# Optimization experiments

Measured on AMD Instinct MI355X. Metric: run time of the kernel, lower is better.

The kernel has to match this reference:

```python
import jax, jax.numpy as jnp
import numpy as np

NH = 16
D = 1024
B, T = 4, 4096


def setup_inputs() -> dict:
    key = jax.random.key(0)
    k1, k2, k3, k4 = jax.random.split(key, 4)
    x = jax.random.normal(k1, (B, T, D), dtype=jnp.float32)
    phi = jax.random.normal(k2, (B, T), dtype=jnp.float32)
    W_attn = jax.random.normal(k3, (D, D), dtype=jnp.float32) * 0.02
    W_proj = jax.random.normal(k4, (D, D), dtype=jnp.float32) * 0.02
    gamma = jnp.ones((NH, 1), dtype=jnp.float32)
    temp = jnp.ones((NH, 1), dtype=jnp.float32)
    return {"x": x, "phi": phi, "W_attn": W_attn, "W_proj": W_proj,
            "gamma": gamma, "temp": temp}


def reference(x, phi, W_attn, W_proj, gamma, temp):
    Bb, Tt, d = x.shape
    hd = d // NH
    # c_attn (no bias), split heads: [B, nh, T, hd]
    w = (x @ W_attn.T).reshape(Bb, Tt, NH, hd).transpose(0, 2, 1, 3)
    w_sq = w * w
    denom = jnp.maximum(jnp.cumsum(w_sq, axis=-2), 1e-12)
    w_norm = w_sq / denom
    tssa_score = w_norm.sum(-1) * temp                       # [B, nh, T]
    phi_Q = phi[:, None, :]                                  # [B, 1, T]
    steps = jnp.arange(1, Tt + 1, dtype=x.dtype)
    mean_phi = jnp.cumsum(phi, axis=-1)[:, None, :] / steps  # running mean of phi
    penalty = (phi_Q - mean_phi) ** 2                        # [B, 1, T]
    score = tssa_score - gamma * penalty                     # [B, nh, T]
    alpha = jax.nn.softmax(score, axis=1)                    # softmax over HEADS (dim=1)
    dots = jnp.cumsum(w_sq * alpha[..., None], axis=-2) / (
        jnp.cumsum(alpha, axis=-1)[..., None] + 1e-8)
    attn = jnp.minimum(1.0 / (1.0 + dots), 10000.0)
    y = -w * alpha[..., None] * attn                          # [B, nh, T, hd]
    y = y.transpose(0, 2, 1, 3).reshape(Bb, Tt, d)
    y = y @ W_proj.T                                          # dropout is identity (p=0 / eval)
    return (y, alpha)
```

## Files before the change

kernel.cpp:

```cpp
#include <hip/hip_runtime.h>
#include <hip/hip_bf16.h>
#include <stdint.h>

#define NHh 16
#define Dm  1024
#define HD  64
#define Bb  4
#define Tt  4096
#define NCH 128
#define CHL 32

#define BM 256
#define BN 256
#define BK 64
#define NKT (Dm / BK)

using bf16 = __hip_bfloat16;
typedef __attribute__((ext_vector_type(8))) short short8;
typedef __attribute__((ext_vector_type(4))) float f32x4;

__device__ __forceinline__ float bf2f(bf16 v) { return __bfloat162float(v); }

__device__ __forceinline__ float b2f(unsigned short u) {
  union { unsigned int i; float f; } x; x.i = ((unsigned int)u) << 16; return x.f;
}

__device__ __forceinline__ float frcp(float x) {
  float r; asm("v_rcp_f32 %0, %1" : "=v"(r) : "v"(x)); return r;
}

__device__ __forceinline__ void gld_lds16(const void* g, void* l) {
  __builtin_amdgcn_global_load_lds(
      (const __attribute__((address_space(1))) unsigned int*)g,
      (__attribute__((address_space(3))) unsigned int*)l, 16, 0, 0);
}

template <bool OUT_BF16, bool WRITE_S1>
__global__ __launch_bounds__(512, 2) void gemm256(const bf16* __restrict__ A,
                                                  const bf16* __restrict__ W,
                                                  void* __restrict__ Cout,
                                                  float* __restrict__ S1,
                                                  int M, int N, int K) {
  extern __shared__ char smem[];
  const int tid  = threadIdx.x;
  const int lane = tid & 63;
  const int wave = tid >> 6;
  const int bid = blockIdx.x;
  const int swz = (bid & 7) * 32 + (bid >> 3);
  const int bn = (swz & 3) * BN;
  const int bm = (swz >> 2) * BM;
  const int wm = (wave >> 1) * 64;
  const int wn = (wave & 1) * 128;
  const int quad = lane >> 4;
  const int l16  = lane & 15;

  const int srow = wave * 8 + (lane >> 3);
  const int scol = (((lane & 7) ^ (lane >> 3)) << 3);

  const bf16* Abase = A + (size_t)(bm + srow) * K + scol;
  const bf16* Wbase = W + (size_t)(bn + srow) * K + scol;

  f32x4 acc[4][8] = {};

#define SLAB_A(buf, n) (smem + (buf) * 65536 + (n) * 8192 + wave * 1024)
#define SLAB_B(buf, n) (smem + (buf) * 65536 + 32768 + (n) * 8192 + wave * 1024)
#define STAGE_A(buf, n, k0) gld_lds16(Abase + (size_t)(n) * 64 * K + (k0), SLAB_A(buf, n))
#define STAGE_B(buf, n, k0) gld_lds16(Wbase + (size_t)(n) * 64 * K + (k0), SLAB_B(buf, n))
#define LD_FRAG(base, r, s) (*(const short8*)((base) + (size_t)(r) * 128 + ((((s) ^ ((r) & 7))) << 4)))

  STAGE_A(0, 0, 0); STAGE_A(0, 1, 0); STAGE_A(0, 2, 0); STAGE_A(0, 3, 0);
  STAGE_B(0, 0, 0); STAGE_B(0, 1, 0); STAGE_B(0, 2, 0); STAGE_B(0, 3, 0);
  asm volatile("s_waitcnt vmcnt(0)" ::: "memory");
  __builtin_amdgcn_s_barrier();
  __builtin_amdgcn_sched_barrier(0);

  short8 af[4][2], bfv[4][2];
  for (int t = 0; t < NKT; t++) {
    const int buf = t & 1;
    const char* aL = smem + buf * 65536;
    const char* bL = aL + 32768;
    const int k0n = (t + 1) * BK;
    const bool pf = (t + 1 < NKT);

    if (pf) {
      STAGE_A(buf ^ 1, 0, k0n); STAGE_A(buf ^ 1, 1, k0n);
      STAGE_A(buf ^ 1, 2, k0n); STAGE_A(buf ^ 1, 3, k0n);
      STAGE_B(buf ^ 1, 0, k0n); STAGE_B(buf ^ 1, 2, k0n);
    }
#pragma unroll
    for (int mi = 0; mi < 4; mi++) {
      const int r = wm + mi * 16 + l16;
      af[mi][0] = LD_FRAG(aL, r, quad);
      af[mi][1] = LD_FRAG(aL, r, quad + 4);
    }
#pragma unroll
    for (int nj = 0; nj < 4; nj++) {
      const int r = wn + nj * 16 + l16;
      bfv[nj][0] = LD_FRAG(bL, r, quad);
      bfv[nj][1] = LD_FRAG(bL, r, quad + 4);
    }
    __builtin_amdgcn_s_setprio(1);
#pragma unroll
    for (int mi = 0; mi < 4; mi++)
#pragma unroll
      for (int nj = 0; nj < 4; nj++) {
        acc[mi][nj] = __builtin_amdgcn_mfma_f32_16x16x32_bf16(af[mi][0], bfv[nj][0], acc[mi][nj], 0, 0, 0);
        acc[mi][nj] = __builtin_amdgcn_mfma_f32_16x16x32_bf16(af[mi][1], bfv[nj][1], acc[mi][nj], 0, 0, 0);
      }
    __builtin_amdgcn_s_setprio(0);
    if (pf) { asm volatile("s_waitcnt vmcnt(6)" ::: "memory"); }
    else    { asm volatile("s_waitcnt vmcnt(0)" ::: "memory"); }
    __builtin_amdgcn_s_barrier();
    __builtin_amdgcn_sched_barrier(0);

    if (pf) { STAGE_B(buf ^ 1, 1, k0n); STAGE_B(buf ^ 1, 3, k0n); }
#pragma unroll
    for (int nj = 0; nj < 4; nj++) {
      const int r = wn + 64 + nj * 16 + l16;
      bfv[nj][0] = LD_FRAG(bL, r, quad);
      bfv[nj][1] = LD_FRAG(bL, r, quad + 4);
    }
    __builtin_amdgcn_s_setprio(1);
#pragma unroll
    for (int mi = 0; mi < 4; mi++)
#pragma unroll
      for (int nj = 0; nj < 4; nj++) {
        acc[mi][nj + 4] = __builtin_amdgcn_mfma_f32_16x16x32_bf16(af[mi][0], bfv[nj][0], acc[mi][nj + 4], 0, 0, 0);
        acc[mi][nj + 4] = __builtin_amdgcn_mfma_f32_16x16x32_bf16(af[mi][1], bfv[nj][1], acc[mi][nj + 4], 0, 0, 0);
      }
    __builtin_amdgcn_s_setprio(0);
    asm volatile("s_waitcnt vmcnt(2)" ::: "memory");
    __builtin_amdgcn_s_barrier();
    __builtin_amdgcn_sched_barrier(0);
  }

  if constexpr (OUT_BF16) {
    ushort* cst = (ushort*)smem;
#pragma unroll
    for (int nj = 0; nj < 8; nj++) {
      const int gcol = bn + wn + nj * 16 + l16;
      float ss0 = 0.f, ss1 = 0.f;
#pragma unroll
      for (int mi = 0; mi < 4; mi++) {
        float csum = 0.f;
#pragma unroll
        for (int r = 0; r < 4; r++) {
          const int row = wm + mi * 16 + quad * 4 + r;
          const int col = wn + nj * 16 + l16;
          const bf16 hv = __float2bfloat16(acc[mi][nj][r]);
          cst[(row * 512 + ((col * 2) ^ ((row & 7) << 4))) >> 1] = __bfloat16_as_ushort(hv);
          if constexpr (WRITE_S1) { const float fv = bf2f(hv); csum += fv * fv; }
        }
        if constexpr (WRITE_S1) { if (mi < 2) ss0 += csum; else ss1 += csum; }
      }
      if constexpr (WRITE_S1) {
        ss0 += __shfl_xor(ss0, 16, 64); ss0 += __shfl_xor(ss0, 32, 64);
        ss1 += __shfl_xor(ss1, 16, 64); ss1 += __shfl_xor(ss1, 32, 64);
        if (quad == 0) {
          const int h = gcol >> 6, d = gcol & 63;
          const int r0 = bm + wm;
          const int b  = r0 >> 12;
          const int c0 = (r0 & (Tt - 1)) >> 5;
          float* s1p = S1 + (((size_t)(b * NHh + h) * NCH) + c0) * HD + d;
          s1p[0]  = ss0;
          s1p[HD] = ss1;
        }
      }
    }
    asm volatile("s_waitcnt lgkmcnt(0)" ::: "memory");
    __builtin_amdgcn_s_barrier();
#pragma unroll
    for (int it = 0; it < 16; it++) {
      const int idx = it * 512 + tid;
      const int row = idx >> 5;
      const int ch  = idx & 31;
      const short8 v = *(const short8*)(smem + row * 512 + ((ch ^ (row & 7)) << 4));
      *(short8*)((bf16*)Cout + (size_t)(bm + row) * N + bn + ch * 8) = v;
    }
  } else {
#pragma unroll
    for (int nj = 0; nj < 8; nj++) {
      const int col = bn + wn + nj * 16 + l16;
#pragma unroll
      for (int mi = 0; mi < 4; mi++)
#pragma unroll
        for (int r = 0; r < 4; r++) {
          const int row = bm + wm + mi * 16 + quad * 4 + r;
          ((float*)Cout)[(size_t)row * N + col] = acc[mi][nj][r];
        }
    }
  }
#undef SLAB_A
#undef SLAB_B
#undef STAGE_A
#undef STAGE_B
#undef LD_FRAG
}

__global__ __launch_bounds__(256) void prep(const float* __restrict__ x,
                                            const float* __restrict__ Wa,
                                            const float* __restrict__ Wp,
                                            const float* __restrict__ phi,
                                            bf16* __restrict__ x_bf,
                                            bf16* __restrict__ Wa_bf,
                                            bf16* __restrict__ Wp_bf,
                                            float* __restrict__ penalty) {
  const int bid = blockIdx.x;
  if (bid < 1536) {
    const float* in;
    bf16* out;
    int n, nblk, b0;
    if (bid < 1024)      { in = x;  out = x_bf;  n = Bb * Tt * Dm; nblk = 1024; b0 = 0; }
    else if (bid < 1280) { in = Wa; out = Wa_bf; n = Dm * Dm;      nblk = 256;  b0 = 1024; }
    else                 { in = Wp; out = Wp_bf; n = Dm * Dm;      nblk = 256;  b0 = 1280; }
    const int stride = nblk * 256;
    for (int i = (bid - b0) * 256 + threadIdx.x; i * 4 < n; i += stride) {
      const float4 v = *(const float4*)(in + (size_t)i * 4);
      ushort4 o;
      o.x = __bfloat16_as_ushort(__float2bfloat16(v.x));
      o.y = __bfloat16_as_ushort(__float2bfloat16(v.y));
      o.z = __bfloat16_as_ushort(__float2bfloat16(v.z));
      o.w = __bfloat16_as_ushort(__float2bfloat16(v.w));
      *(ushort4*)(out + (size_t)i * 4) = o;
    }
  } else {
    const int b = bid - 1536;
    const int tid = threadIdx.x;
    const int lane = tid & 63, wid = tid >> 6;
    __shared__ float wsum[4];
    __shared__ float carry_s;
    if (tid == 0) carry_s = 0.f;
    __syncthreads();
    for (int r = 0; r < Tt / 256; r++) {
      const int t = r * 256 + tid;
      const float v = phi[b * Tt + t];
      float incl = v;
#pragma unroll
      for (int off = 1; off < 64; off <<= 1) {
        float nn = __shfl_up(incl, off, 64);
        if (lane >= off) incl += nn;
      }
      if (lane == 63) wsum[wid] = incl;
      __syncthreads();
      float woff = carry_s;
      for (int wpre = 0; wpre < wid; wpre++) woff += wsum[wpre];
      const float csum = woff + incl;
      const float mean = csum / (float)(t + 1);
      const float dphi = v - mean;
      penalty[b * Tt + t] = dphi * dphi;
      __syncthreads();
      if (tid == 0) carry_s += wsum[0] + wsum[1] + wsum[2] + wsum[3];
      __syncthreads();
    }
  }
}

__global__ __launch_bounds__(256) void mid_fused(const bf16* __restrict__ w,
                                                 const float* __restrict__ S1,
                                                 const float* __restrict__ temp,
                                                 const float* __restrict__ gamma,
                                                 const float* __restrict__ penalty,
                                                 float* __restrict__ alpha_f,
                                                 float* __restrict__ S2,
                                                 float* __restrict__ SA) {
  const int c = blockIdx.x, b = blockIdx.y;
  const int tid = threadIdx.x, h = tid >> 4, l = tid & 15;
  __shared__ float sm_t[CHL][NHh + 1];
  __shared__ float sm_a[CHL][NHh + 1];
  __shared__ float sm_g[NHh], sm_tv[NHh];
  if (tid < NHh) { sm_g[tid] = gamma[tid]; sm_tv[tid] = temp[tid]; }

  const float4* p4 = (const float4*)(S1 + (((size_t)(b * NHh + h) * NCH)) * HD + l * 4);
  float4 s0 = {0,0,0,0}, s1v = {0,0,0,0}, s2v = {0,0,0,0}, s3v = {0,0,0,0};
  int cc = 0;
  for (; cc + 4 <= c; cc += 4) {
    const float4 v0 = p4[(size_t)cc * 16];
    const float4 v1 = p4[(size_t)(cc + 1) * 16];
    const float4 v2 = p4[(size_t)(cc + 2) * 16];
    const float4 v3 = p4[(size_t)(cc + 3) * 16];
    s0.x += v0.x; s0.y += v0.y; s0.z += v0.z; s0.w += v0.w;
    s1v.x += v1.x; s1v.y += v1.y; s1v.z += v1.z; s1v.w += v1.w;
    s2v.x += v2.x; s2v.y += v2.y; s2v.z += v2.z; s2v.w += v2.w;
    s3v.x += v3.x; s3v.y += v3.y; s3v.z += v3.z; s3v.w += v3.w;
  }
  for (; cc < c; cc++) {
    const float4 v0 = p4[(size_t)cc * 16];
    s0.x += v0.x; s0.y += v0.y; s0.z += v0.z; s0.w += v0.w;
  }
  float a0 = s0.x + s1v.x + s2v.x + s3v.x;
  float a1 = s0.y + s1v.y + s2v.y + s3v.y;
  float a2 = s0.z + s1v.z + s2v.z + s3v.z;
  float a3 = s0.w + s1v.w + s2v.w + s3v.w;
  __syncthreads();

  const bf16* wp = w + ((size_t)(b * Tt + c * CHL)) * Dm + h * HD + l * 4;
  const float tv = sm_tv[h];
#pragma unroll 8
  for (int i = 0; i < CHL; i++) {
    const ushort4 v = *(const ushort4*)(wp + (size_t)i * Dm);
    const float f0 = b2f(v.x), f1 = b2f(v.y), f2 = b2f(v.z), f3 = b2f(v.w);
    const float q0 = f0 * f0, q1 = f1 * f1, q2 = f2 * f2, q3 = f3 * f3;
    a0 += q0; a1 += q1; a2 += q2; a3 += q3;
    float val = q0 * frcp(fmaxf(a0, 1e-12f)) + q1 * frcp(fmaxf(a1, 1e-12f))
              + q2 * frcp(fmaxf(a2, 1e-12f)) + q3 * frcp(fmaxf(a3, 1e-12f));
    val += __shfl_xor(val, 1, 64);
    val += __shfl_xor(val, 2, 64);
    val += __shfl_xor(val, 4, 64);
    val += __shfl_xor(val, 8, 64);
    if (l == 0) sm_t[i][h] = tv * val;
  }
  __syncthreads();

  if (tid < CHL) {
    const int t = tid;
    const float pen = penalty[(size_t)b * Tt + c * CHL + t];
    float sc[NHh];
    float mx = -1e30f;
#pragma unroll
    for (int hh = 0; hh < NHh; hh++) {
      sc[hh] = sm_t[t][hh] - sm_g[hh] * pen;
      mx = fmaxf(mx, sc[hh]);
    }
    float sum = 0.f;
#pragma unroll
    for (int hh = 0; hh < NHh; hh++) { const float e = __expf(sc[hh] - mx); sc[hh] = e; sum += e; }
    const float inv = 1.f / sum;
#pragma unroll
    for (int hh = 0; hh < NHh; hh++) sm_a[t][hh] = sc[hh] * inv;
  }
  __syncthreads();

#pragma unroll
  for (int k2 = 0; k2 < CHL / 16; k2++) {
    const int t = k2 * 16 + l;
    alpha_f[((size_t)(b * NHh + h)) * Tt + c * CHL + t] = sm_a[t][h];
  }

  float d0 = 0.f, d1 = 0.f, d2 = 0.f, d3 = 0.f, sa = 0.f;
#pragma unroll 8
  for (int i = 0; i < CHL; i++) {
    const float a = sm_a[i][h];
    const ushort4 v = *(const ushort4*)(wp + (size_t)i * Dm);
    const float f0 = b2f(v.x), f1 = b2f(v.y), f2 = b2f(v.z), f3 = b2f(v.w);
    d0 += f0 * f0 * a; d1 += f1 * f1 * a; d2 += f2 * f2 * a; d3 += f3 * f3 * a;
    sa += a;
  }
  float4 o; o.x = d0; o.y = d1; o.z = d2; o.w = d3;
  *(float4*)&S2[(((size_t)(b * NHh + h) * NCH) + c) * HD + l * 4] = o;
  if (l == 0) SA[(size_t)(b * NHh + h) * NCH + c] = sa;
}

__global__ __launch_bounds__(256) void y_phase3(const bf16* __restrict__ w,
                                                const float* __restrict__ alpha_f,
                                                const float* __restrict__ S2,
                                                const float* __restrict__ SA,
                                                bf16* __restrict__ yprime) {
  const int c = blockIdx.x, b = blockIdx.y;
  const int tid = threadIdx.x, h = tid >> 4, l = tid & 15;

  const float* sap = SA + (size_t)(b * NHh + h) * NCH;
  float sa_part = 0.f;
  for (int cc = l; cc < c; cc += 16) sa_part += sap[cc];
  sa_part += __shfl_xor(sa_part, 1, 64);
  sa_part += __shfl_xor(sa_part, 2, 64);
  sa_part += __shfl_xor(sa_part, 4, 64);
  sa_part += __shfl_xor(sa_part, 8, 64);
  float acca = sa_part;

  const float4* p4 = (const float4*)(S2 + (((size_t)(b * NHh + h) * NCH)) * HD + l * 4);
  float4 s0 = {0,0,0,0}, s1v = {0,0,0,0}, s2v = {0,0,0,0}, s3v = {0,0,0,0};
  int cc = 0;
  for (; cc + 4 <= c; cc += 4) {
    const float4 v0 = p4[(size_t)cc * 16];
    const float4 v1 = p4[(size_t)(cc + 1) * 16];
    const float4 v2 = p4[(size_t)(cc + 2) * 16];
    const float4 v3 = p4[(size_t)(cc + 3) * 16];
    s0.x += v0.x; s0.y += v0.y; s0.z += v0.z; s0.w += v0.w;
    s1v.x += v1.x; s1v.y += v1.y; s1v.z += v1.z; s1v.w += v1.w;
    s2v.x += v2.x; s2v.y += v2.y; s2v.z += v2.z; s2v.w += v2.w;
    s3v.x += v3.x; s3v.y += v3.y; s3v.z += v3.z; s3v.w += v3.w;
  }
  for (; cc < c; cc++) {
    const float4 v0 = p4[(size_t)cc * 16];
    s0.x += v0.x; s0.y += v0.y; s0.z += v0.z; s0.w += v0.w;
  }
  float a0 = s0.x + s1v.x + s2v.x + s3v.x;
  float a1 = s0.y + s1v.y + s2v.y + s3v.y;
  float a2 = s0.z + s1v.z + s2v.z + s3v.z;
  float a3 = s0.w + s1v.w + s2v.w + s3v.w;

  const bf16* wp = w + ((size_t)(b * Tt + c * CHL)) * Dm + h * HD + l * 4;
  const float* ap = alpha_f + (size_t)(b * NHh + h) * Tt + c * CHL;
  bf16* yp = yprime + ((size_t)(b * Tt + c * CHL)) * Dm + h * HD + l * 4;
#pragma unroll 8
  for (int i = 0; i < CHL; i++) {
    const float a = ap[i];
    const ushort4 v = *(const ushort4*)(wp + (size_t)i * Dm);
    const float f0 = b2f(v.x), f1 = b2f(v.y), f2 = b2f(v.z), f3 = b2f(v.w);
    a0 += f0 * f0 * a; a1 += f1 * f1 * a; a2 += f2 * f2 * a; a3 += f3 * f3 * a;
    acca += a;
    const float rinv = frcp(acca + 1e-8f);
    const float at0 = fminf(frcp(1.f + a0 * rinv), 10000.f);
    const float at1 = fminf(frcp(1.f + a1 * rinv), 10000.f);
    const float at2 = fminf(frcp(1.f + a2 * rinv), 10000.f);
    const float at3 = fminf(frcp(1.f + a3 * rinv), 10000.f);
    ushort4 o;
    o.x = __bfloat16_as_ushort(__float2bfloat16(-f0 * a * at0));
    o.y = __bfloat16_as_ushort(__float2bfloat16(-f1 * a * at1));
    o.z = __bfloat16_as_ushort(__float2bfloat16(-f2 * a * at2));
    o.w = __bfloat16_as_ushort(__float2bfloat16(-f3 * a * at3));
    *(ushort4*)(yp + (size_t)i * Dm) = o;
  }
}

extern "C" void kernel_launch(void* const* d_in, const int* in_sizes, int n_in,
                              void* d_out, int out_size, void* d_ws, size_t ws_size,
                              hipStream_t stream) {
  const float* x     = (const float*)d_in[0];
  const float* phi   = (const float*)d_in[1];
  const float* Wattn = (const float*)d_in[2];
  const float* Wproj = (const float*)d_in[3];
  const float* gamma = (const float*)d_in[4];
  const float* temp  = (const float*)d_in[5];

  float* y_out    = (float*)d_out;
  float* alpha_f  = y_out + (size_t)Bb * Tt * Dm;

  char* ws = (char*)d_ws;
  bf16*  x_bf   = (bf16*)ws;  ws += (size_t)Bb * Tt * Dm * 2;
  bf16*  Wa_bf  = (bf16*)ws;  ws += (size_t)Dm * Dm * 2;
  bf16*  Wp_bf  = (bf16*)ws;  ws += (size_t)Dm * Dm * 2;
  bf16*  w_bf   = (bf16*)ws;  ws += (size_t)Bb * Tt * Dm * 2;
  float* pen    = (float*)ws; ws += (size_t)Bb * Tt * 4;
  float* S1     = (float*)ws; ws += (size_t)Bb * NHh * NCH * HD * 4;
  float* S2     = (float*)ws; ws += (size_t)Bb * NHh * NCH * HD * 4;
  float* SA     = (float*)ws; ws += (size_t)Bb * NHh * NCH * 4;
  bf16*  yprime = x_bf;

  static int attr_done = 0;
  if (!attr_done) {
    hipFuncSetAttribute((const void*)gemm256<true, true>,
                        hipFuncAttributeMaxDynamicSharedMemorySize, 131072);
    hipFuncSetAttribute((const void*)gemm256<false, false>,
                        hipFuncAttributeMaxDynamicSharedMemorySize, 131072);
    attr_done = 1;
  }

  const int M = Bb * Tt, N = Dm, K = Dm;
  dim3 gg((M / BM) * (N / BN)), gb(512);

  prep<<<dim3(1540), dim3(256), 0, stream>>>(x, Wattn, Wproj, phi, x_bf, Wa_bf, Wp_bf, pen);
  gemm256<true, true><<<gg, gb, 131072, stream>>>(x_bf, Wa_bf, (void*)w_bf, S1, M, N, K);
  mid_fused<<<dim3(NCH, Bb), dim3(256), 0, stream>>>(w_bf, S1, temp, gamma, pen,
                                                     alpha_f, S2, SA);
  y_phase3<<<dim3(NCH, Bb), dim3(256), 0, stream>>>(w_bf, alpha_f, S2, SA, yprime);
  gemm256<false, false><<<gg, gb, 131072, stream>>>(yprime, Wp_bf, (void*)y_out, nullptr, M, N, K);
}
```

Baseline: 253.5 us.

## Widen mid and phase3 kernels to 1024 threads with LDS-staged w chunk

Both middle kernels now launch 1024 threads per block, with one thread per column instead of four columns per thread. Each block first copies its 32x1024 bf16 chunk of w into shared memory with direct global-to-LDS loads, and both passes then read w from shared memory rather than re-reading global memory. This quadruples the parallelism across the 512 blocks and removes the duplicate global read of w in mid_fused. In exchange it adds 64KB of dynamic LDS per block, two more shuffle steps in each reduction, and scalar (non-vectorised) S1/S2 prefix loads.

```diff
diff --git a/kernel.cpp b/kernel.cpp
--- a/kernel.cpp
+++ b/kernel.cpp
@@ -255,58 +255,57 @@
   }
 }
 
-__global__ __launch_bounds__(256) void mid_fused(const bf16* __restrict__ w,
-                                                 const float* __restrict__ S1,
-                                                 const float* __restrict__ temp,
-                                                 const float* __restrict__ gamma,
-                                                 const float* __restrict__ penalty,
-                                                 float* __restrict__ alpha_f,
-                                                 float* __restrict__ S2,
-                                                 float* __restrict__ SA) {
-  const int c = blockIdx.x, b = blockIdx.y;
-  const int tid = threadIdx.x, h = tid >> 4, l = tid & 15;
+__global__ __launch_bounds__(1024, 8) void mid_fused(const bf16* __restrict__ w,
+                                                     const float* __restrict__ S1,
+                                                     const float* __restrict__ temp,
+                                                     const float* __restrict__ gamma,
+                                                     const float* __restrict__ penalty,
+                                                     float* __restrict__ alpha_f,
+                                                     float* __restrict__ S2,
+                                                     float* __restrict__ SA) {
+  extern __shared__ ushort wlds[];
   __shared__ float sm_t[CHL][NHh + 1];
   __shared__ float sm_a[CHL][NHh + 1];
   __shared__ float sm_g[NHh], sm_tv[NHh];
+  const int c = blockIdx.x, b = blockIdx.y;
+  const int tid = threadIdx.x;
+  const int h = tid >> 6, l = tid & 63;
+
+  {
+    const char* g = (const char*)(w + ((size_t)(b * Tt + c * CHL)) * Dm) + h * 4096 + l * 16;
+    char* d = (char*)wlds + h * 4096;
+    gld_lds16(g, d); gld_lds16(g + 1024, d + 1024);
+    gld_lds16(g + 2048, d + 2048); gld_lds16(g + 3072, d + 3072);
+  }
   if (tid < NHh) { sm_g[tid] = gamma[tid]; sm_tv[tid] = temp[tid]; }
 
-  const float4* p4 = (const float4*)(S1 + (((size_t)(b * NHh + h) * NCH)) * HD + l * 4);
-  float4 s0 = {0,0,0,0}, s1v = {0,0,0,0}, s2v = {0,0,0,0}, s3v = {0,0,0,0};
+  const float* p = S1 + ((size_t)(b * NHh + h) * NCH) * HD + l;
+  float s0 = 0.f, s1 = 0.f, s2 = 0.f, s3 = 0.f;
   int cc = 0;
   for (; cc + 4 <= c; cc += 4) {
-    const float4 v0 = p4[(size_t)cc * 16];
-    const float4 v1 = p4[(size_t)(cc + 1) * 16];
-    const float4 v2 = p4[(size_t)(cc + 2) * 16];
-    const float4 v3 = p4[(size_t)(cc + 3) * 16];
-    s0.x += v0.x; s0.y += v0.y; s0.z += v0.z; s0.w += v0.w;
-    s1v.x += v1.x; s1v.y += v1.y; s1v.z += v1.z; s1v.w += v1.w;
-    s2v.x += v2.x; s2v.y += v2.y; s2v.z += v2.z; s2v.w += v2.w;
-    s3v.x += v3.x; s3v.y += v3.y; s3v.z += v3.z; s3v.w += v3.w;
-  }
-  for (; cc < c; cc++) {
-    const float4 v0 = p4[(size_t)cc * 16];
-    s0.x += v0.x; s0.y += v0.y; s0.z += v0.z; s0.w += v0.w;
-  }
-  float a0 = s0.x + s1v.x + s2v.x + s3v.x;
-  float a1 = s0.y + s1v.y + s2v.y + s3v.y;
-  float a2 = s0.z + s1v.z + s2v.z + s3v.z;
-  float a3 = s0.w + s1v.w + s2v.w + s3v.w;
+    s0 += p[(size_t)cc * HD];       s1 += p[(size_t)(cc + 1) * HD];
+    s2 += p[(size_t)(cc + 2) * HD]; s3 += p[(size_t)(cc + 3) * HD];
+  }
+  for (; cc < c; cc++) s0 += p[(size_t)cc * HD];
+  float a = s0 + s1 + s2 + s3;
+
+  asm volatile("s_waitcnt vmcnt(0)" ::: "memory");
   __syncthreads();
 
-  const bf16* wp = w + ((size_t)(b * Tt + c * CHL)) * Dm + h * HD + l * 4;
   const float tv = sm_tv[h];
-#pragma unroll 8
+  const int col = h * 64 + l;
+#pragma unroll 4
   for (int i = 0; i < CHL; i++) {
-    const ushort4 v = *(const ushort4*)(wp + (size_t)i * Dm);
-    const float f0 = b2f(v.x), f1 = b2f(v.y), f2 = b2f(v.z), f3 = b2f(v.w);
-    const float q0 = f0 * f0, q1 = f1 * f1, q2 = f2 * f2, q3 = f3 * f3;
-    a0 += q0; a1 += q1; a2 += q2; a3 += q3;
-    float val = q0 * frcp(fmaxf(a0, 1e-12f)) + q1 * frcp(fmaxf(a1, 1e-12f))
-              + q2 * frcp(fmaxf(a2, 1e-12f)) + q3 * frcp(fmaxf(a3, 1e-12f));
+    const float f = b2f(wlds[i * Dm + col]);
+    const float q = f * f;
+    a += q;
+    float val = q * frcp(fmaxf(a, 1e-12f));
     val += __shfl_xor(val, 1, 64);
     val += __shfl_xor(val, 2, 64);
     val += __shfl_xor(val, 4, 64);
     val += __shfl_xor(val, 8, 64);
+    val += __shfl_xor(val, 16, 64);
+    val += __shfl_xor(val, 32, 64);
     if (l == 0) sm_t[i][h] = tv * val;
   }
   __syncthreads();
@@ -330,86 +329,77 @@
   }
   __syncthreads();
 
-#pragma unroll
-  for (int k2 = 0; k2 < CHL / 16; k2++) {
-    const int t = k2 * 16 + l;
-    alpha_f[((size_t)(b * NHh + h)) * Tt + c * CHL + t] = sm_a[t][h];
-  }
-
-  float d0 = 0.f, d1 = 0.f, d2 = 0.f, d3 = 0.f, sa = 0.f;
-#pragma unroll 8
+  if (l < CHL) alpha_f[((size_t)(b * NHh + h)) * Tt + c * CHL + l] = sm_a[l][h];
+
+  float dsum = 0.f, sa = 0.f;
+#pragma unroll 4
   for (int i = 0; i < CHL; i++) {
-    const float a = sm_a[i][h];
-    const ushort4 v = *(const ushort4*)(wp + (size_t)i * Dm);
-    const float f0 = b2f(v.x), f1 = b2f(v.y), f2 = b2f(v.z), f3 = b2f(v.w);
-    d0 += f0 * f0 * a; d1 += f1 * f1 * a; d2 += f2 * f2 * a; d3 += f3 * f3 * a;
-    sa += a;
-  }
-  float4 o; o.x = d0; o.y = d1; o.z = d2; o.w = d3;
-  *(float4*)&S2[(((size_t)(b * NHh + h) * NCH) + c) * HD + l * 4] = o;
+    const float al = sm_a[i][h];
+    const float f = b2f(wlds[i * Dm + col]);
+    dsum += f * f * al;
+    sa += al;
+  }
+  S2[(((size_t)(b * NHh + h) * NCH) + c) * HD + l] = dsum;
   if (l == 0) SA[(size_t)(b * NHh + h) * NCH + c] = sa;
 }
 
-__global__ __launch_bounds__(256) void y_phase3(const bf16* __restrict__ w,
-                                                const float* __restrict__ alpha_f,
-                                                const float* __restrict__ S2,
-                                                const float* __restrict__ SA,
-                                                bf16* __restrict__ yprime) {
+__global__ __launch_bounds__(1024, 8) void y_phase3(const bf16* __restrict__ w,
+                                                    const float* __restrict__ alpha_f,
+                                                    const float* __restrict__ S2,
+                                                    const float* __restrict__ SA,
+                                                    bf16* __restrict__ yprime) {
+  extern __shared__ ushort wlds[];
+  __shared__ float sm_al[NHh][CHL];
   const int c = blockIdx.x, b = blockIdx.y;
-  const int tid = threadIdx.x, h = tid >> 4, l = tid & 15;
+  const int tid = threadIdx.x;
+  const int h = tid >> 6, l = tid & 63;
+
+  {
+    const char* g = (const char*)(w + ((size_t)(b * Tt + c * CHL)) * Dm) + h * 4096 + l * 16;
+    char* d = (char*)wlds + h * 4096;
+    gld_lds16(g, d); gld_lds16(g + 1024, d + 1024);
+    gld_lds16(g + 2048, d + 2048); gld_lds16(g + 3072, d + 3072);
+  }
+  if (tid < NHh * CHL) {
+    const int h2 = tid >> 5, t = tid & 31;
+    sm_al[h2][t] = alpha_f[((size_t)(b * NHh + h2)) * Tt + c * CHL + t];
+  }
 
   const float* sap = SA + (size_t)(b * NHh + h) * NCH;
   float sa_part = 0.f;
-  for (int cc = l; cc < c; cc += 16) sa_part += sap[cc];
+  for (int cc = l; cc < c; cc += 64) sa_part += sap[cc];
   sa_part += __shfl_xor(sa_part, 1, 64);
   sa_part += __shfl_xor(sa_part, 2, 64);
   sa_part += __shfl_xor(sa_part, 4, 64);
   sa_part += __shfl_xor(sa_part, 8, 64);
+  sa_part += __shfl_xor(sa_part, 16, 64);
+  sa_part += __shfl_xor(sa_part, 32, 64);
   float acca = sa_part;
 
-  const float4* p4 = (const float4*)(S2 + (((size_t)(b * NHh + h) * NCH)) * HD + l * 4);
-  float4 s0 = {0,0,0,0}, s1v = {0,0,0,0}, s2v = {0,0,0,0}, s3v = {0,0,0,0};
+  const float* p = S2 + ((size_t)(b * NHh + h) * NCH) * HD + l;
+  float s0 = 0.f, s1 = 0.f, s2 = 0.f, s3 = 0.f;
   int cc = 0;
   for (; cc + 4 <= c; cc += 4) {
-    const float4 v0 = p4[(size_t)cc * 16];
-    const float4 v1 = p4[(size_t)(cc + 1) * 16];
-    const float4 v2 = p4[(size_t)(cc + 2) * 16];
-    const float4 v3 = p4[(size_t)(cc + 3) * 16];
-    s0.x += v0.x; s0.y += v0.y; s0.z += v0.z; s0.w += v0.w;
-    s1v.x += v1.x; s1v.y += v1.y; s1v.z += v1.z; s1v.w += v1.w;
-    s2v.x += v2.x; s2v.y += v2.y; s2v.z += v2.z; s2v.w += v2.w;
-    s3v.x += v3.x; s3v.y += v3.y; s3v.z += v3.z; s3v.w += v3.w;
-  }
-  for (; cc < c; cc++) {
-    const float4 v0 = p4[(size_t)cc * 16];
-    s0.x += v0.x; s0.y += v0.y; s0.z += v0.z; s0.w += v0.w;
-  }
-  float a0 = s0.x + s1v.x + s2v.x + s3v.x;
-  float a1 = s0.y + s1v.y + s2v.y + s3v.y;
-  float a2 = s0.z + s1v.z + s2v.z + s3v.z;
-  float a3 = s0.w + s1v.w + s2v.w + s3v.w;
-
-  const bf16* wp = w + ((size_t)(b * Tt + c * CHL)) * Dm + h * HD + l * 4;
-  const float* ap = alpha_f + (size_t)(b * NHh + h) * Tt + c * CHL;
-  bf16* yp = yprime + ((size_t)(b * Tt + c * CHL)) * Dm + h * HD + l * 4;
-#pragma unroll 8
+    s0 += p[(size_t)cc * HD];       s1 += p[(size_t)(cc + 1) * HD];
+    s2 += p[(size_t)(cc + 2) * HD]; s3 += p[(size_t)(cc + 3) * HD];
+  }
+  for (; cc < c; cc++) s0 += p[(size_t)cc * HD];
+  float a = s0 + s1 + s2 + s3;
+
+  asm volatile("s_waitcnt vmcnt(0)" ::: "memory");
+  __syncthreads();
+
+  const int col = h * 64 + l;
+  bf16* yp = yprime + ((size_t)(b * Tt + c * CHL)) * Dm + col;
+#pragma unroll 4
   for (int i = 0; i < CHL; i++) {
-    const float a = ap[i];
-    const ushort4 v = *(const ushort4*)(wp + (size_t)i * Dm);
-    const float f0 = b2f(v.x), f1 = b2f(v.y), f2 = b2f(v.z), f3 = b2f(v.w);
-    a0 += f0 * f0 * a; a1 += f1 * f1 * a; a2 += f2 * f2 * a; a3 += f3 * f3 * a;
-    acca += a;
+    const float al = sm_al[h][i];
+    const float f = b2f(wlds[i * Dm + col]);
+    a += f * f * al;
+    acca += al;
     const float rinv = frcp(acca + 1e-8f);
-    const float at0 = fminf(frcp(1.f + a0 * rinv), 10000.f);
-    const float at1 = fminf(frcp(1.f + a1 * rinv), 10000.f);
-    const float at2 = fminf(frcp(1.f + a2 * rinv), 10000.f);
-    const float at3 = fminf(frcp(1.f + a3 * rinv), 10000.f);
-    ushort4 o;
-    o.x = __bfloat16_as_ushort(__float2bfloat16(-f0 * a * at0));
-    o.y = __bfloat16_as_ushort(__float2bfloat16(-f1 * a * at1));
-    o.z = __bfloat16_as_ushort(__float2bfloat16(-f2 * a * at2));
-    o.w = __bfloat16_as_ushort(__float2bfloat16(-f3 * a * at3));
-    *(ushort4*)(yp + (size_t)i * Dm) = o;
+    const float attn = fminf(frcp(1.f + a * rinv), 10000.f);
+    yp[(size_t)i * Dm] = __float2bfloat16(-f * al * attn);
   }
 }
 
@@ -443,6 +433,10 @@
                         hipFuncAttributeMaxDynamicSharedMemorySize, 131072);
     hipFuncSetAttribute((const void*)gemm256<false, false>,
                         hipFuncAttributeMaxDynamicSharedMemorySize, 131072);
+    hipFuncSetAttribute((const void*)mid_fused,
+                        hipFuncAttributeMaxDynamicSharedMemorySize, 65536);
+    hipFuncSetAttribute((const void*)y_phase3,
+                        hipFuncAttributeMaxDynamicSharedMemorySize, 65536);
     attr_done = 1;
   }
 
@@ -451,8 +445,8 @@
 
   prep<<<dim3(1540), dim3(256), 0, stream>>>(x, Wattn, Wproj, phi, x_bf, Wa_bf, Wp_bf, pen);
   gemm256<true, true><<<gg, gb, 131072, stream>>>(x_bf, Wa_bf, (void*)w_bf, S1, M, N, K);
-  mid_fused<<<dim3(NCH, Bb), dim3(256), 0, stream>>>(w_bf, S1, temp, gamma, pen,
-                                                     alpha_f, S2, SA);
-  y_phase3<<<dim3(NCH, Bb), dim3(256), 0, stream>>>(w_bf, alpha_f, S2, SA, yprime);
+  mid_fused<<<dim3(NCH, Bb), dim3(1024), 65536, stream>>>(w_bf, S1, temp, gamma, pen,
+                                                          alpha_f, S2, SA);
+  y_phase3<<<dim3(NCH, Bb), dim3(1024), 65536, stream>>>(w_bf, alpha_f, S2, SA, yprime);
   gemm256<false, false><<<gg, gb, 131072, stream>>>(yprime, Wp_bf, (void*)y_out, nullptr, M, N, K);
 }
```

After: 262.9 us. 3.7% more time.
